# Optimization experiments

Hardware: AMD Instinct MI355X
Metric: run time of the kernel (lower is better)

The kernel has to match this reference:

```python
import jax, jax.numpy as jnp
import numpy as np

N, E, D, L, R, G, C = 50000, 800000, 64, 3, 2, 128, 10


def setup_inputs() -> dict:
    key = jax.random.key(0)
    ks = jax.random.split(key, 16)
    s = 0.05
    x = jax.random.normal(ks[0], (N, D), dtype=jnp.float32)
    edge_index = jax.random.randint(ks[1], (2, E), 0, N, dtype=jnp.int64)
    edge_type = jax.random.randint(ks[2], (E,), 0, R, dtype=jnp.int64)
    batch = jnp.sort(jax.random.randint(ks[3], (N,), 0, G, dtype=jnp.int64))
    # per-layer self-loop Linear, per-(layer,relation) GIN eps + 2-layer MLP
    self_W = jax.random.normal(ks[4], (L, D, D), dtype=jnp.float32) * s
    self_b = jax.random.normal(ks[5], (L, D), dtype=jnp.float32) * s
    eps = jnp.zeros((L, R), dtype=jnp.float32)  # eps=0, train_eps=True
    mlp_W1 = jax.random.normal(ks[6], (L, R, D, D), dtype=jnp.float32) * s
    mlp_b1 = jax.random.normal(ks[7], (L, R, D), dtype=jnp.float32) * s
    mlp_W2 = jax.random.normal(ks[8], (L, R, D, D), dtype=jnp.float32) * s
    mlp_b2 = jax.random.normal(ks[9], (L, R, D), dtype=jnp.float32) * s
    lin1_W = jax.random.normal(ks[10], (D, D), dtype=jnp.float32) * s
    lin1_b = jax.random.normal(ks[11], (D,), dtype=jnp.float32) * s
    lin2_W = jax.random.normal(ks[12], (D, C), dtype=jnp.float32) * s
    lin2_b = jax.random.normal(ks[13], (C,), dtype=jnp.float32) * s
    return {"x": x, "edge_index": edge_index, "edge_type": edge_type, "batch": batch,
            "self_W": self_W, "self_b": self_b, "eps": eps,
            "mlp_W1": mlp_W1, "mlp_b1": mlp_b1, "mlp_W2": mlp_W2, "mlp_b2": mlp_b2,
            "lin1_W": lin1_W, "lin1_b": lin1_b, "lin2_W": lin2_W, "lin2_b": lin2_b}


def reference(x, edge_index, edge_type, batch, self_W, self_b, eps,
              mlp_W1, mlp_b1, mlp_W2, mlp_b2, lin1_W, lin1_b, lin2_W, lin2_b):
    src, dst = edge_index[0], edge_index[1]
    h = x
    for l in range(L):
        x_new = h @ self_W[l] + self_b[l]
        x_src = h[src]  # [E, D] gather of source features, done once per layer
        for r in range(R):
            # per-relation edge masking + scatter-add aggregation
            msg = jnp.where((edge_type == r)[:, None], x_src, jnp.zeros((), h.dtype))
            agg = jax.ops.segment_sum(msg, dst, num_segments=N)  # [N, D]
            z = (1.0 + eps[l, r]) * h + agg  # GIN combine
            z = jax.nn.relu(z @ mlp_W1[l, r] + mlp_b1[l, r])
            x_new = x_new + (z @ mlp_W2[l, r] + mlp_b2[l, r])
        h = x_new
    # global mean pooling over graphs
    sums = jax.ops.segment_sum(h, batch, num_segments=G)  # [G, D]
    counts = jax.ops.segment_sum(jnp.ones((N,), h.dtype), batch, num_segments=G)
    pooled = sums / jnp.maximum(counts, 1.0)[:, None]
    out = jax.nn.relu(pooled @ lin1_W + lin1_b)
    # dropout omitted (eval mode)
    out = out @ lin2_W + lin2_b
    return out
```

## Files before the change

kernel.cpp:

```cpp
#include <hip/hip_runtime.h>

#define Nn 50000
#define Dd 64
#define Ee 800000
#define Ll 3
#define Rr 2
#define Gg 128
#define Cc 10
#define NR (Nn * Rr)
#define NB ((NR + 1023) / 1024)
#define NT (Nn / 16)

typedef __attribute__((ext_vector_type(8))) short short8;
typedef __attribute__((ext_vector_type(4))) float f32x4;

__device__ __forceinline__ unsigned short bf16_rne(float x) {
  unsigned u = __float_as_uint(x);
  unsigned r = u + 0x7fffu + ((u >> 16) & 1u);
  return (unsigned short)(r >> 16);
}
__device__ __forceinline__ float bf16_tof(unsigned short b) {
  return __uint_as_float(((unsigned)b) << 16);
}
__device__ __forceinline__ void acc8(float* z, uint4 u) {
  z[0] += __uint_as_float(u.x << 16);
  z[1] += __uint_as_float(u.x & 0xffff0000u);
  z[2] += __uint_as_float(u.y << 16);
  z[3] += __uint_as_float(u.y & 0xffff0000u);
  z[4] += __uint_as_float(u.z << 16);
  z[5] += __uint_as_float(u.z & 0xffff0000u);
  z[6] += __uint_as_float(u.w << 16);
  z[7] += __uint_as_float(u.w & 0xffff0000u);
}

__global__ __launch_bounds__(256) void k_hist(
    const int* __restrict__ dst, const int* __restrict__ et,
    int* __restrict__ counts)
{
  int e = blockIdx.x * 256 + threadIdx.x;
  if (e >= Ee) return;
  atomicAdd(&counts[et[e] * Nn + dst[e]], 1);
}

__global__ __launch_bounds__(1024) void k_scan1(
    const int* __restrict__ counts, int* __restrict__ offs,
    int* __restrict__ btot)
{
  __shared__ int s[1024];
  int i = blockIdx.x * 1024 + threadIdx.x;
  int v = (i < NR) ? counts[i] : 0;
  s[threadIdx.x] = v;
  __syncthreads();
#pragma unroll
  for (int d = 1; d < 1024; d <<= 1) {
    int t = (threadIdx.x >= d) ? s[threadIdx.x - d] : 0;
    __syncthreads();
    s[threadIdx.x] += t;
    __syncthreads();
  }
  if (i < NR) offs[i + 1] = s[threadIdx.x];
  if (threadIdx.x == 1023) btot[blockIdx.x] = s[1023];
}

__global__ __launch_bounds__(128) void k_scan2(
    const int* __restrict__ btot, int* __restrict__ bscan)
{
  __shared__ int s[128];
  int v = (threadIdx.x < NB) ? btot[threadIdx.x] : 0;
  s[threadIdx.x] = v;
  __syncthreads();
#pragma unroll
  for (int d = 1; d < 128; d <<= 1) {
    int t = (threadIdx.x >= d) ? s[threadIdx.x - d] : 0;
    __syncthreads();
    s[threadIdx.x] += t;
    __syncthreads();
  }
  if (threadIdx.x < NB) bscan[threadIdx.x] = s[threadIdx.x] - v;
}

__global__ __launch_bounds__(1024) void k_scan3(
    const int* __restrict__ counts, const int* __restrict__ bscan,
    int* __restrict__ offs, int* __restrict__ cursor)
{
  int i = blockIdx.x * 1024 + threadIdx.x;
  if (i >= NR) return;
  int o = offs[i + 1] + bscan[blockIdx.x];
  offs[i + 1] = o;
  cursor[i] = o - counts[i];
  if (i == 0) offs[0] = 0;
}

__global__ __launch_bounds__(256) void k_fill(
    const int* __restrict__ src, const int* __restrict__ dst,
    const int* __restrict__ et, int* __restrict__ cursor,
    int* __restrict__ elist)
{
  int e = blockIdx.x * 256 + threadIdx.x;
  if (e >= Ee) return;
  int pos = atomicAdd(&cursor[et[e] * Nn + dst[e]], 1);
  elist[pos] = src[e];
}

__global__ __launch_bounds__(256) void k_cvt(
    const float* __restrict__ x, unsigned short* __restrict__ hb)
{
  int i = blockIdx.x * 256 + threadIdx.x;
  if (i >= (Nn * Dd) / 4) return;
  const float4 v = *(const float4*)&x[(size_t)i * 4];
  ushort4 o;
  o.x = bf16_rne(v.x); o.y = bf16_rne(v.y);
  o.z = bf16_rne(v.z); o.w = bf16_rne(v.w);
  *(ushort4*)&hb[(size_t)i * 4] = o;
}

__global__ __launch_bounds__(256) void k_prep(
    const float* __restrict__ selfW, const float* __restrict__ W1,
    const float* __restrict__ W2, unsigned short* __restrict__ wtHi,
    unsigned short* __restrict__ wtLo)
{
  int i = blockIdx.x * 256 + threadIdx.x;
  if (i >= Ll * 5 * 4096) return;
  int l = i / (5 * 4096);
  int rem = i - l * 5 * 4096;
  int m = rem >> 12;
  int e = rem & 4095;
  int k = e >> 6, c = e & 63;
  const float* p;
  if (m == 0)      p = selfW + (size_t)l * 4096;
  else if (m == 1) p = W1 + ((size_t)l * 2 + 0) * 4096;
  else if (m == 2) p = W2 + ((size_t)l * 2 + 0) * 4096;
  else if (m == 3) p = W1 + ((size_t)l * 2 + 1) * 4096;
  else             p = W2 + ((size_t)l * 2 + 1) * 4096;
  float w = p[e];
  unsigned short hi = bf16_rne(w);
  unsigned short lo = bf16_rne(w - bf16_tof(hi));
  size_t o = ((size_t)(l * 5 + m) * 64 + c) * 64 + k;
  wtHi[o] = hi;
  wtLo[o] = lo;
}

#define WOFF(m, c, ks) ((size_t)(m)*4096 + (size_t)(c)*64 + (ks)*32 + koff)

__global__ __launch_bounds__(128, 5) void k_update(
    const float* __restrict__ h, const unsigned short* __restrict__ hb,
    const int* __restrict__ offs, const int* __restrict__ elist,
    const unsigned short* __restrict__ wtHi, const unsigned short* __restrict__ wtLo,
    const float* __restrict__ selfb, const float* __restrict__ eps,
    const float* __restrict__ b1, const float* __restrict__ b2,
    float* __restrict__ hn, unsigned short* __restrict__ hnb, int l)
{
  __shared__ __align__(16) unsigned short tbh[2][16 * 72];
  __shared__ __align__(16) unsigned short tbl[2][16 * 72];
  __shared__ float xfer[16 * 65];
  const int wave = threadIdx.x >> 6;
  const int lane = threadIdx.x & 63;
  const int task = blockIdx.x;
  const int r = wave;
  const int idx15 = lane & 15;
  const int kg = lane >> 4;
  const int koff = kg * 8;
  const int nodeA = task * 16 + idx15;

  float f[2][8];
  {
    const float* hp = &h[(size_t)nodeA * 64 + koff];
    const float4 a0 = *(const float4*)(hp);
    const float4 a1 = *(const float4*)(hp + 4);
    const float4 b0 = *(const float4*)(hp + 32);
    const float4 b1v = *(const float4*)(hp + 36);
    f[0][0] = a0.x; f[0][1] = a0.y; f[0][2] = a0.z; f[0][3] = a0.w;
    f[0][4] = a1.x; f[0][5] = a1.y; f[0][6] = a1.z; f[0][7] = a1.w;
    f[1][0] = b0.x; f[1][1] = b0.y; f[1][2] = b0.z; f[1][3] = b0.w;
    f[1][4] = b1v.x; f[1][5] = b1v.y; f[1][6] = b1v.z; f[1][7] = b1v.w;
  }

  const unsigned short* whi = wtHi + (size_t)l * 5 * 4096;
  const unsigned short* wlo = wtLo + (size_t)l * 5 * 4096;
  const int m1 = 1 + 2 * r, m2 = 2 + 2 * r;
  const float er = 1.0f + eps[l * Rr + r];

  float za[2][8];
#pragma unroll
  for (int ks = 0; ks < 2; ++ks)
#pragma unroll
    for (int j = 0; j < 8; ++j) za[ks][j] = 0.0f;
  {
    int aidx = r * Nn + nodeA;
    int jb = offs[aidx], je = offs[aidx + 1];
    int j = jb;
    for (; j + 3 < je; j += 4) {
      int s0 = elist[j], s1 = elist[j + 1], s2 = elist[j + 2], s3 = elist[j + 3];
      const unsigned short* q0 = &hb[(size_t)s0 * 64 + koff];
      const unsigned short* q1 = &hb[(size_t)s1 * 64 + koff];
      const unsigned short* q2 = &hb[(size_t)s2 * 64 + koff];
      const unsigned short* q3 = &hb[(size_t)s3 * 64 + koff];
      const uint4 a0 = *(const uint4*)(q0);
      const uint4 a1 = *(const uint4*)(q1);
      const uint4 a2 = *(const uint4*)(q2);
      const uint4 a3 = *(const uint4*)(q3);
      const uint4 b0 = *(const uint4*)(q0 + 32);
      const uint4 b1q = *(const uint4*)(q1 + 32);
      const uint4 b2q = *(const uint4*)(q2 + 32);
      const uint4 b3 = *(const uint4*)(q3 + 32);
      acc8(za[0], a0); acc8(za[0], a1); acc8(za[0], a2); acc8(za[0], a3);
      acc8(za[1], b0); acc8(za[1], b1q); acc8(za[1], b2q); acc8(za[1], b3);
    }
    for (; j < je; ++j) {
      const unsigned short* q = &hb[(size_t)elist[j] * 64 + koff];
      const uint4 a = *(const uint4*)(q);
      const uint4 b = *(const uint4*)(q + 32);
      acc8(za[0], a); acc8(za[1], b);
    }
  }

  short8 zhi[2], zlo[2];
#pragma unroll
  for (int ks = 0; ks < 2; ++ks)
#pragma unroll
    for (int j = 0; j < 8; ++j) {
      float zf = er * f[ks][j] + za[ks][j];
      unsigned short hb2 = bf16_rne(zf);
      zhi[ks][j] = (short)hb2;
      zlo[ks][j] = (short)bf16_rne(zf - bf16_tof(hb2));
    }

  f32x4 tacc[4];
#pragma unroll
  for (int cb = 0; cb < 4; ++cb) {
    float bi = b1[((size_t)l * 2 + r) * 64 + cb * 16 + idx15];
    tacc[cb] = (f32x4){bi, bi, bi, bi};
  }
#pragma unroll
  for (int cb = 0; cb < 4; ++cb) {
    int c = cb * 16 + idx15;
#pragma unroll
    for (int ks = 0; ks < 2; ++ks) {
      const short8 bh = *(const short8*)&whi[WOFF(m1, c, ks)];
      const short8 bl = *(const short8*)&wlo[WOFF(m1, c, ks)];
      tacc[cb] = __builtin_amdgcn_mfma_f32_16x16x32_bf16(zhi[ks], bh, tacc[cb], 0, 0, 0);
      tacc[cb] = __builtin_amdgcn_mfma_f32_16x16x32_bf16(zhi[ks], bl, tacc[cb], 0, 0, 0);
      tacc[cb] = __builtin_amdgcn_mfma_f32_16x16x32_bf16(zlo[ks], bh, tacc[cb], 0, 0, 0);
    }
  }
#pragma unroll
  for (int cb = 0; cb < 4; ++cb)
#pragma unroll
    for (int q = 0; q < 4; ++q) {
      float tv = fmaxf(tacc[cb][q], 0.0f);
      unsigned short hb2 = bf16_rne(tv);
      tbh[wave][(kg * 4 + q) * 72 + cb * 16 + idx15] = hb2;
      tbl[wave][(kg * 4 + q) * 72 + cb * 16 + idx15] = bf16_rne(tv - bf16_tof(hb2));
    }
  asm volatile("s_waitcnt lgkmcnt(0)" ::: "memory");
  __builtin_amdgcn_sched_barrier(0);
  short8 thi[2], tlo[2];
#pragma unroll
  for (int ks = 0; ks < 2; ++ks) {
    thi[ks] = *(const short8*)&tbh[wave][idx15 * 72 + ks * 32 + koff];
    tlo[ks] = *(const short8*)&tbl[wave][idx15 * 72 + ks * 32 + koff];
  }

  f32x4 facc[4];
#pragma unroll
  for (int cb = 0; cb < 4; ++cb) {
    int c = cb * 16 + idx15;
    float bi = b2[((size_t)l * 2 + r) * 64 + c];
    if (wave == 1) bi += selfb[l * 64 + c];
    facc[cb] = (f32x4){bi, bi, bi, bi};
  }
#pragma unroll
  for (int cb = 0; cb < 4; ++cb) {
    int c = cb * 16 + idx15;
#pragma unroll
    for (int ks = 0; ks < 2; ++ks) {
      const short8 bh = *(const short8*)&whi[WOFF(m2, c, ks)];
      const short8 bl = *(const short8*)&wlo[WOFF(m2, c, ks)];
      facc[cb] = __builtin_amdgcn_mfma_f32_16x16x32_bf16(thi[ks], bh, facc[cb], 0, 0, 0);
      facc[cb] = __builtin_amdgcn_mfma_f32_16x16x32_bf16(thi[ks], bl, facc[cb], 0, 0, 0);
      facc[cb] = __builtin_amdgcn_mfma_f32_16x16x32_bf16(tlo[ks], bh, facc[cb], 0, 0, 0);
    }
  }
  if (wave == 1) {
    short8 ahi[2], alo[2];
#pragma unroll
    for (int ks = 0; ks < 2; ++ks)
#pragma unroll
      for (int j = 0; j < 8; ++j) {
        unsigned short hb2 = bf16_rne(f[ks][j]);
        ahi[ks][j] = (short)hb2;
        alo[ks][j] = (short)bf16_rne(f[ks][j] - bf16_tof(hb2));
      }
#pragma unroll
    for (int cb = 0; cb < 4; ++cb) {
      int c = cb * 16 + idx15;
#pragma unroll
      for (int ks = 0; ks < 2; ++ks) {
        const short8 bh = *(const short8*)&whi[WOFF(0, c, ks)];
        const short8 bl = *(const short8*)&wlo[WOFF(0, c, ks)];
        facc[cb] = __builtin_amdgcn_mfma_f32_16x16x32_bf16(ahi[ks], bh, facc[cb], 0, 0, 0);
        facc[cb] = __builtin_amdgcn_mfma_f32_16x16x32_bf16(ahi[ks], bl, facc[cb], 0, 0, 0);
        facc[cb] = __builtin_amdgcn_mfma_f32_16x16x32_bf16(alo[ks], bh, facc[cb], 0, 0, 0);
      }
    }
#pragma unroll
    for (int cb = 0; cb < 4; ++cb)
#pragma unroll
      for (int q = 0; q < 4; ++q)
        xfer[(kg * 4 + q) * 65 + cb * 16 + idx15] = facc[cb][q];
  }
  __syncthreads();
  if (wave == 0) {
#pragma unroll
    for (int cb = 0; cb < 4; ++cb)
#pragma unroll
      for (int q = 0; q < 4; ++q) {
        int row = kg * 4 + q, col = cb * 16 + idx15;
        float v = facc[cb][q] + xfer[row * 65 + col];
        size_t o = ((size_t)task * 16 + row) * 64 + col;
        hn[o] = v;
        hnb[o] = bf16_rne(v);
      }
  }
}

__global__ __launch_bounds__(256) void k_pool(
    const float* __restrict__ h, const int* __restrict__ batch,
    float* __restrict__ sums, float* __restrict__ cnts)
{
  int w = blockIdx.x * 4 + (threadIdx.x >> 6);
  int lane = threadIdx.x & 63;
  int start = w * 64;
  if (start >= Nn) return;
  int cnt = min(64, Nn - start);
  int bg = batch[min(start + lane, Nn - 1)];
  int cur = __shfl(bg, 0, 64);
  float acc = 0.0f;
  int run = 0;
  for (int i = 0; i < cnt; ++i) {
    int g = __shfl(bg, i, 64);
    float v = h[(size_t)(start + i) * 64 + lane];
    if (g != cur) {
      atomicAdd(&sums[(size_t)cur * 64 + lane], acc);
      if (lane == 0) atomicAdd(&cnts[cur], (float)run);
      acc = 0.0f; run = 0; cur = g;
    }
    acc += v; run++;
  }
  atomicAdd(&sums[(size_t)cur * 64 + lane], acc);
  if (lane == 0) atomicAdd(&cnts[cur], (float)run);
}

__global__ __launch_bounds__(256) void k_head(
    const float* __restrict__ sums, const float* __restrict__ cnts,
    const float* __restrict__ l1W, const float* __restrict__ l1b,
    const float* __restrict__ l2W, const float* __restrict__ l2b,
    float* __restrict__ out)
{
  int wave = threadIdx.x >> 6;
  int lane = threadIdx.x & 63;
  int g = blockIdx.x * 4 + wave;
  if (g >= Gg) return;
  float p = sums[(size_t)g * Dd + lane] / fmaxf(cnts[g], 1.0f);
  float t = l1b[lane];
#pragma unroll
  for (int k = 0; k < Dd; ++k)
    t += __shfl(p, k, 64) * l1W[k * Dd + lane];
  t = fmaxf(t, 0.0f);
  float o = (lane < Cc) ? l2b[lane] : 0.0f;
#pragma unroll
  for (int k = 0; k < Dd; ++k) {
    float w = (lane < Cc) ? l2W[k * Cc + lane] : 0.0f;
    o += __shfl(t, k, 64) * w;
  }
  if (lane < Cc) out[(size_t)g * Cc + lane] = o;
}

extern "C" void kernel_launch(void* const* d_in, const int* in_sizes, int n_in,
                              void* d_out, int out_size, void* d_ws, size_t ws_size,
                              hipStream_t stream)
{
  const float* x     = (const float*)d_in[0];
  const int*   ei    = (const int*)d_in[1];
  const int*   et    = (const int*)d_in[2];
  const int*   batch = (const int*)d_in[3];
  const float* selfW = (const float*)d_in[4];
  const float* selfb = (const float*)d_in[5];
  const float* eps   = (const float*)d_in[6];
  const float* W1    = (const float*)d_in[7];
  const float* b1    = (const float*)d_in[8];
  const float* W2    = (const float*)d_in[9];
  const float* b2    = (const float*)d_in[10];
  const float* l1W   = (const float*)d_in[11];
  const float* l1b   = (const float*)d_in[12];
  const float* l2W   = (const float*)d_in[13];
  const float* l2b   = (const float*)d_in[14];
  float* out = (float*)d_out;

  float* buf0 = (float*)d_ws;
  float* buf1 = buf0 + (size_t)Nn * Dd;
  unsigned short* hb0 = (unsigned short*)(buf1 + (size_t)Nn * Dd);
  unsigned short* hb1 = hb0 + (size_t)Nn * Dd;
  float* sums = (float*)(hb1 + (size_t)Nn * Dd);
  float* cnts = sums + (size_t)Gg * Dd;
  unsigned short* wtHi = (unsigned short*)(cnts + Gg);
  unsigned short* wtLo = wtHi + (size_t)Ll * 5 * 4096;
  int* counts = (int*)(wtLo + (size_t)Ll * 5 * 4096);
  int* offs   = counts + NR;
  int* cursor = offs + NR + 1;
  int* btot   = cursor + NR;
  int* bscan  = btot + NB;
  int* elist  = bscan + NB;

  const int* src = ei;
  const int* dst = ei + Ee;

  hipMemsetAsync(sums, 0, (size_t)(Gg * Dd + Gg) * sizeof(float), stream);
  hipMemsetAsync(counts, 0, (size_t)NR * sizeof(int), stream);
  k_prep<<<(Ll * 5 * 4096 + 255) / 256, 256, 0, stream>>>(selfW, W1, W2, wtHi, wtLo);
  k_cvt<<<(Nn * Dd / 4 + 255) / 256, 256, 0, stream>>>(x, hb0);

  k_hist<<<(Ee + 255) / 256, 256, 0, stream>>>(dst, et, counts);
  k_scan1<<<NB, 1024, 0, stream>>>(counts, offs, btot);
  k_scan2<<<1, 128, 0, stream>>>(btot, bscan);
  k_scan3<<<NB, 1024, 0, stream>>>(counts, bscan, offs, cursor);
  k_fill<<<(Ee + 255) / 256, 256, 0, stream>>>(src, dst, et, cursor, elist);

  const float* h = x;
  const unsigned short* hbc = hb0;
  float* hn = buf0;
  unsigned short* hnb = hb1;
  for (int l = 0; l < Ll; ++l) {
    k_update<<<NT, 128, 0, stream>>>(h, hbc, offs, elist, wtHi, wtLo,
                                     selfb, eps, b1, b2, hn, hnb, l);
    h = hn;
    hbc = hnb;
    hn = (hn == buf0) ? buf1 : buf0;
    hnb = (hnb == hb0) ? hb1 : hb0;
  }
  k_pool<<<(Nn / 64 + 4) / 4, 256, 0, stream>>>(h, batch, sums, cnts);
  k_head<<<32, 256, 0, stream>>>(sums, cnts, l1W, l1b, l2W, l2b, out);
}
```

Before: 296.8 us.

## Fuse setup kernels, merge pool with head, alias LDS to raise occupancy

Merges the bf16 conversion, weight prep and edge histogram into one launch split by block ranges. Pooling and the MLP head become a single kernel with one block per graph, which finds its node range by binary search over the sorted batch array, so the atomics and the memset go away. In the update kernel the xfer buffer now reuses the tile LDS behind an extra barrier, and the occupancy hint rises from 5 to 8 blocks per CU. In exchange, pooling runs on only 128 blocks with serial per-graph sums, and the higher occupancy hint may force register spills.

```diff
diff --git a/kernel.cpp b/kernel.cpp
--- a/kernel.cpp
+++ b/kernel.cpp
@@ -11,6 +11,10 @@
 #define NB ((NR + 1023) / 1024)
 #define NT (Nn / 16)
 
+#define CVT_B  3125
+#define PREP_B 240
+#define HIST_B 3125
+
 typedef __attribute__((ext_vector_type(8))) short short8;
 typedef __attribute__((ext_vector_type(4))) float f32x4;
 
@@ -33,13 +37,45 @@
   z[7] += __uint_as_float(u.w & 0xffff0000u);
 }
 
-__global__ __launch_bounds__(256) void k_hist(
+__global__ __launch_bounds__(256) void k_setup(
+    const float* __restrict__ x, unsigned short* __restrict__ hb,
+    const float* __restrict__ selfW, const float* __restrict__ W1,
+    const float* __restrict__ W2, unsigned short* __restrict__ wtHi,
+    unsigned short* __restrict__ wtLo,
     const int* __restrict__ dst, const int* __restrict__ et,
     int* __restrict__ counts)
 {
-  int e = blockIdx.x * 256 + threadIdx.x;
-  if (e >= Ee) return;
-  atomicAdd(&counts[et[e] * Nn + dst[e]], 1);
+  int b = blockIdx.x;
+  if (b < CVT_B) {
+    int i = b * 256 + threadIdx.x;
+    const float4 v = *(const float4*)&x[(size_t)i * 4];
+    ushort4 o;
+    o.x = bf16_rne(v.x); o.y = bf16_rne(v.y);
+    o.z = bf16_rne(v.z); o.w = bf16_rne(v.w);
+    *(ushort4*)&hb[(size_t)i * 4] = o;
+  } else if (b < CVT_B + PREP_B) {
+    int i = (b - CVT_B) * 256 + threadIdx.x;
+    int l = i / (5 * 4096);
+    int rem = i - l * 5 * 4096;
+    int m = rem >> 12;
+    int e = rem & 4095;
+    int k = e >> 6, c = e & 63;
+    const float* p;
+    if (m == 0)      p = selfW + (size_t)l * 4096;
+    else if (m == 1) p = W1 + ((size_t)l * 2 + 0) * 4096;
+    else if (m == 2) p = W2 + ((size_t)l * 2 + 0) * 4096;
+    else if (m == 3) p = W1 + ((size_t)l * 2 + 1) * 4096;
+    else             p = W2 + ((size_t)l * 2 + 1) * 4096;
+    float w = p[e];
+    unsigned short hi = bf16_rne(w);
+    unsigned short lo = bf16_rne(w - bf16_tof(hi));
+    size_t o = ((size_t)(l * 5 + m) * 64 + c) * 64 + k;
+    wtHi[o] = hi;
+    wtLo[o] = lo;
+  } else {
+    int e = (b - CVT_B - PREP_B) * 256 + threadIdx.x;
+    atomicAdd(&counts[et[e] * Nn + dst[e]], 1);
+  }
 }
 
 __global__ __launch_bounds__(1024) void k_scan1(
@@ -102,47 +138,9 @@
   elist[pos] = src[e];
 }
 
-__global__ __launch_bounds__(256) void k_cvt(
-    const float* __restrict__ x, unsigned short* __restrict__ hb)
-{
-  int i = blockIdx.x * 256 + threadIdx.x;
-  if (i >= (Nn * Dd) / 4) return;
-  const float4 v = *(const float4*)&x[(size_t)i * 4];
-  ushort4 o;
-  o.x = bf16_rne(v.x); o.y = bf16_rne(v.y);
-  o.z = bf16_rne(v.z); o.w = bf16_rne(v.w);
-  *(ushort4*)&hb[(size_t)i * 4] = o;
-}
-
-__global__ __launch_bounds__(256) void k_prep(
-    const float* __restrict__ selfW, const float* __restrict__ W1,
-    const float* __restrict__ W2, unsigned short* __restrict__ wtHi,
-    unsigned short* __restrict__ wtLo)
-{
-  int i = blockIdx.x * 256 + threadIdx.x;
-  if (i >= Ll * 5 * 4096) return;
-  int l = i / (5 * 4096);
-  int rem = i - l * 5 * 4096;
-  int m = rem >> 12;
-  int e = rem & 4095;
-  int k = e >> 6, c = e & 63;
-  const float* p;
-  if (m == 0)      p = selfW + (size_t)l * 4096;
-  else if (m == 1) p = W1 + ((size_t)l * 2 + 0) * 4096;
-  else if (m == 2) p = W2 + ((size_t)l * 2 + 0) * 4096;
-  else if (m == 3) p = W1 + ((size_t)l * 2 + 1) * 4096;
-  else             p = W2 + ((size_t)l * 2 + 1) * 4096;
-  float w = p[e];
-  unsigned short hi = bf16_rne(w);
-  unsigned short lo = bf16_rne(w - bf16_tof(hi));
-  size_t o = ((size_t)(l * 5 + m) * 64 + c) * 64 + k;
-  wtHi[o] = hi;
-  wtLo[o] = lo;
-}
-
 #define WOFF(m, c, ks) ((size_t)(m)*4096 + (size_t)(c)*64 + (ks)*32 + koff)
 
-__global__ __launch_bounds__(128, 5) void k_update(
+__global__ __launch_bounds__(128, 8) void k_update(
     const float* __restrict__ h, const unsigned short* __restrict__ hb,
     const int* __restrict__ offs, const int* __restrict__ elist,
     const unsigned short* __restrict__ wtHi, const unsigned short* __restrict__ wtLo,
@@ -152,7 +150,7 @@
 {
   __shared__ __align__(16) unsigned short tbh[2][16 * 72];
   __shared__ __align__(16) unsigned short tbl[2][16 * 72];
-  __shared__ float xfer[16 * 65];
+  float* xfer = (float*)&tbh[0][0];
   const int wave = threadIdx.x >> 6;
   const int lane = threadIdx.x & 63;
   const int task = blockIdx.x;
@@ -303,6 +301,9 @@
         facc[cb] = __builtin_amdgcn_mfma_f32_16x16x32_bf16(alo[ks], bh, facc[cb], 0, 0, 0);
       }
     }
+  }
+  __syncthreads();
+  if (wave == 1) {
 #pragma unroll
     for (int cb = 0; cb < 4; ++cb)
 #pragma unroll
@@ -324,44 +325,33 @@
   }
 }
 
-__global__ __launch_bounds__(256) void k_pool(
+__global__ __launch_bounds__(64) void k_poolhead(
     const float* __restrict__ h, const int* __restrict__ batch,
-    float* __restrict__ sums, float* __restrict__ cnts)
-{
-  int w = blockIdx.x * 4 + (threadIdx.x >> 6);
-  int lane = threadIdx.x & 63;
-  int start = w * 64;
-  if (start >= Nn) return;
-  int cnt = min(64, Nn - start);
-  int bg = batch[min(start + lane, Nn - 1)];
-  int cur = __shfl(bg, 0, 64);
-  float acc = 0.0f;
-  int run = 0;
-  for (int i = 0; i < cnt; ++i) {
-    int g = __shfl(bg, i, 64);
-    float v = h[(size_t)(start + i) * 64 + lane];
-    if (g != cur) {
-      atomicAdd(&sums[(size_t)cur * 64 + lane], acc);
-      if (lane == 0) atomicAdd(&cnts[cur], (float)run);
-      acc = 0.0f; run = 0; cur = g;
-    }
-    acc += v; run++;
-  }
-  atomicAdd(&sums[(size_t)cur * 64 + lane], acc);
-  if (lane == 0) atomicAdd(&cnts[cur], (float)run);
-}
-
-__global__ __launch_bounds__(256) void k_head(
-    const float* __restrict__ sums, const float* __restrict__ cnts,
     const float* __restrict__ l1W, const float* __restrict__ l1b,
     const float* __restrict__ l2W, const float* __restrict__ l2b,
     float* __restrict__ out)
 {
-  int wave = threadIdx.x >> 6;
-  int lane = threadIdx.x & 63;
-  int g = blockIdx.x * 4 + wave;
-  if (g >= Gg) return;
-  float p = sums[(size_t)g * Dd + lane] / fmaxf(cnts[g], 1.0f);
+  int g = blockIdx.x;
+  int lane = threadIdx.x;
+  int lo = 0, hi = Nn;
+  while (lo < hi) { int mid = (lo + hi) >> 1; if (batch[mid] < g) lo = mid + 1; else hi = mid; }
+  int start = lo;
+  hi = Nn;
+  while (lo < hi) { int mid = (lo + hi) >> 1; if (batch[mid] < g + 1) lo = mid + 1; else hi = mid; }
+  int end = lo;
+
+  float acc = 0.0f;
+  int i = start;
+  for (; i + 3 < end; i += 4) {
+    float v0 = h[(size_t)i * 64 + lane];
+    float v1 = h[(size_t)(i + 1) * 64 + lane];
+    float v2 = h[(size_t)(i + 2) * 64 + lane];
+    float v3 = h[(size_t)(i + 3) * 64 + lane];
+    acc += (v0 + v1) + (v2 + v3);
+  }
+  for (; i < end; ++i) acc += h[(size_t)i * 64 + lane];
+  float p = acc / fmaxf((float)(end - start), 1.0f);
+
   float t = l1b[lane];
 #pragma unroll
   for (int k = 0; k < Dd; ++k)
@@ -401,9 +391,7 @@
   float* buf1 = buf0 + (size_t)Nn * Dd;
   unsigned short* hb0 = (unsigned short*)(buf1 + (size_t)Nn * Dd);
   unsigned short* hb1 = hb0 + (size_t)Nn * Dd;
-  float* sums = (float*)(hb1 + (size_t)Nn * Dd);
-  float* cnts = sums + (size_t)Gg * Dd;
-  unsigned short* wtHi = (unsigned short*)(cnts + Gg);
+  unsigned short* wtHi = hb1 + (size_t)Nn * Dd;
   unsigned short* wtLo = wtHi + (size_t)Ll * 5 * 4096;
   int* counts = (int*)(wtLo + (size_t)Ll * 5 * 4096);
   int* offs   = counts + NR;
@@ -415,12 +403,10 @@
   const int* src = ei;
   const int* dst = ei + Ee;
 
-  hipMemsetAsync(sums, 0, (size_t)(Gg * Dd + Gg) * sizeof(float), stream);
   hipMemsetAsync(counts, 0, (size_t)NR * sizeof(int), stream);
-  k_prep<<<(Ll * 5 * 4096 + 255) / 256, 256, 0, stream>>>(selfW, W1, W2, wtHi, wtLo);
-  k_cvt<<<(Nn * Dd / 4 + 255) / 256, 256, 0, stream>>>(x, hb0);
-
-  k_hist<<<(Ee + 255) / 256, 256, 0, stream>>>(dst, et, counts);
+  k_setup<<<CVT_B + PREP_B + HIST_B, 256, 0, stream>>>(
+      x, hb0, selfW, W1, W2, wtHi, wtLo, dst, et, counts);
+
   k_scan1<<<NB, 1024, 0, stream>>>(counts, offs, btot);
   k_scan2<<<1, 128, 0, stream>>>(btot, bscan);
   k_scan3<<<NB, 1024, 0, stream>>>(counts, bscan, offs, cursor);
@@ -438,6 +424,5 @@
     hn = (hn == buf0) ? buf1 : buf0;
     hnb = (hnb == hb0) ? hb1 : hb0;
   }
-  k_pool<<<(Nn / 64 + 4) / 4, 256, 0, stream>>>(h, batch, sums, cnts);
-  k_head<<<32, 256, 0, stream>>>(sums, cnts, l1W, l1b, l2W, l2b, out);
-}
+  k_poolhead<<<Gg, 64, 0, stream>>>(h, batch, l1W, l1b, l2W, l2b, out);
+}
```

After: 335.2 us. +13.0%, slower.
